# Kernel tuning notes

Hardware: AMD Instinct MI355X
Metric: run time of the kernel (lower is better)

The kernel has to match this reference:

```python
import jax, jax.numpy as jnp
import numpy as np

B, S, H = 2, 2048, 2048
NUM_HEADS, HEAD_DIM, GROUP_SIZE = 16, 128, 4
NUM_KV_HEADS = NUM_HEADS // GROUP_SIZE
ROPE_THETA = 10000.0


def setup_inputs() -> dict:
    key = jax.random.key(0)
    ks = jax.random.split(key, 10)
    xavier = lambda k, fi, fo: jax.random.uniform(k, (fi, fo), jnp.float32,
                                                  -jnp.sqrt(6.0 / (fi + fo)), jnp.sqrt(6.0 / (fi + fo)))
    hidden_states = jax.random.normal(ks[0], (B, S, H), jnp.float32)
    # causal mask: 1.0 where attention is disallowed (strictly upper triangle)
    mask = jnp.triu(jnp.ones((S, S), jnp.float32), k=1)[None, None, :, :]
    mask = jnp.broadcast_to(mask, (B, 1, S, S))
    return {
        "hidden_states": hidden_states,
        "mask": mask,
        "Wq": xavier(ks[1], H, NUM_HEADS * HEAD_DIM), "bq": jnp.zeros((NUM_HEADS * HEAD_DIM,), jnp.float32),
        "Wk": xavier(ks[2], H, NUM_KV_HEADS * HEAD_DIM), "bk": jnp.zeros((NUM_KV_HEADS * HEAD_DIM,), jnp.float32),
        "Wv": xavier(ks[3], H, NUM_KV_HEADS * HEAD_DIM), "bv": jnp.zeros((NUM_KV_HEADS * HEAD_DIM,), jnp.float32),
        "Wo": xavier(ks[4], NUM_HEADS * HEAD_DIM, H), "bo": jnp.zeros((H,), jnp.float32),
    }


def _apply_rope(q, k):
    # q: [b, s, hq, d], k: [b, s, hk, d]
    s, d = q.shape[1], q.shape[-1]
    inv_freq = 1.0 / (ROPE_THETA ** (jnp.arange(0, d, 2, dtype=jnp.float32) / d))  # [d/2]
    angles = jnp.arange(s, dtype=jnp.float32)[:, None] * inv_freq[None, :]          # [s, d/2]
    cos = jnp.cos(angles)[None, :, None, :]  # [1, s, 1, d/2]
    sin = jnp.sin(angles)[None, :, None, :]

    def rot(x):
        x1, x2 = jnp.split(x, 2, axis=-1)
        return jnp.concatenate([x1 * cos - x2 * sin, x1 * sin + x2 * cos], axis=-1)

    return rot(q), rot(k)


def reference(hidden_states, mask, Wq, bq, Wk, bk, Wv, bv, Wo, bo):
    b, s, _ = hidden_states.shape
    scale = 1.0 / jnp.sqrt(jnp.float32(HEAD_DIM))

    q = (hidden_states @ Wq + bq).reshape(b, s, NUM_HEADS, HEAD_DIM)
    k = (hidden_states @ Wk + bk).reshape(b, s, NUM_KV_HEADS, HEAD_DIM)
    v = (hidden_states @ Wv + bv).reshape(b, s, NUM_KV_HEADS, HEAD_DIM)

    q, k = _apply_rope(q, k)

    q = jnp.transpose(q, (0, 2, 1, 3))  # [b, hq, s, d]
    k = jnp.transpose(k, (0, 2, 1, 3))  # [b, hk, s, d]
    v = jnp.transpose(v, (0, 2, 1, 3))

    new_past_key, new_past_value = k, v

    # GQA: repeat each KV head group_size times
    k_rep = jnp.repeat(k, GROUP_SIZE, axis=1)  # [b, hq, s, d]
    v_rep = jnp.repeat(v, GROUP_SIZE, axis=1)

    attn_scores = jnp.einsum('bhqd,bhkd->bhqk', q, k_rep) * scale  # [b, hq, s, s]
    attn_scores = attn_scores + mask * -1e9
    attn_probs = jax.nn.softmax(attn_scores, axis=-1)
    attn_output = jnp.einsum('bhqk,bhkd->bhqd', attn_probs, v_rep)

    attn_output = attn_output.transpose(0, 2, 1, 3).reshape(b, s, NUM_HEADS * HEAD_DIM)
    attn_output = attn_output @ Wo + bo
    return attn_output, new_past_key, new_past_value
```

## Files before the change

kernel.cpp:

```cpp
#include <hip/hip_runtime.h>
#include <stdint.h>

#define S_LEN 2048
#define HDIM  2048
#define N_HEADS 16
#define HEAD_D 128
#define N_KV 4

typedef unsigned short u16;
typedef __attribute__((ext_vector_type(8))) short bf16x8;
typedef __attribute__((ext_vector_type(4))) short bf16x4;
typedef __attribute__((ext_vector_type(4))) float f32x4;

#define MFMA_PV(a, b, c) __builtin_amdgcn_mfma_f32_16x16x16bf16_1k(a, b, c, 0, 0, 0)

__device__ __forceinline__ u16 f2bf(float f) {
  unsigned u = __float_as_uint(f);
  u += 0x7FFFu + ((u >> 16) & 1u);
  return (u16)(u >> 16);
}

__device__ __forceinline__ float bf2f(u16 v) {
  return __uint_as_float(((unsigned)v) << 16);
}

__device__ __forceinline__ void gll16(void* lds, const void* gp) {
  __builtin_amdgcn_global_load_lds(
      (const __attribute__((address_space(1))) void*)gp,
      (__attribute__((address_space(3))) void*)lds, 16, 0, 0);
}

__global__ __launch_bounds__(256) void k_convert(const float* __restrict__ src,
                                                 u16* __restrict__ dst, int n4) {
  int i = blockIdx.x * 256 + threadIdx.x;
  if (i < n4) {
    float4 v = ((const float4*)src)[i];
    ushort4 o;
    o.x = f2bf(v.x); o.y = f2bf(v.y); o.z = f2bf(v.z); o.w = f2bf(v.w);
    ((ushort4*)dst)[i] = o;
  }
}

__global__ __launch_bounds__(256) void k_transpose_w(const float* __restrict__ W,
                                                     u16* __restrict__ Wt,
                                                     int K, int N) {
  __shared__ float tile[64][65];
  int k0 = blockIdx.x * 64, n0 = blockIdx.y * 64;
  int tr = threadIdx.x >> 6, tc = threadIdx.x & 63;
#pragma unroll
  for (int i = 0; i < 16; ++i) {
    int r = tr + i * 4;
    tile[r][tc] = W[(size_t)(k0 + r) * N + n0 + tc];
  }
  __syncthreads();
#pragma unroll
  for (int i = 0; i < 16; ++i) {
    int r = tr + i * 4;
    Wt[(size_t)(n0 + r) * K + k0 + tc] = f2bf(tile[tc][r]);
  }
}

__device__ __forceinline__ void gemm_tile_128(
    const u16* __restrict__ A, const u16* __restrict__ Bt,
    const float* __restrict__ bias, float* __restrict__ C,
    int m0, int n0, int K, int ldc) {
  __shared__ __align__(16) u16 sA[128 * 32];
  __shared__ __align__(16) u16 sB[128 * 32];
  const int tid = threadIdx.x;
  const int lane = tid & 63;
  const int wave = tid >> 6;
  const int quad = lane >> 4;
  const int l15 = lane & 15;
  const int wm = (wave >> 1) << 6;
  const int wn = (wave & 1) << 6;

  f32x4 acc[4][4];
#pragma unroll
  for (int i = 0; i < 4; ++i)
#pragma unroll
    for (int j = 0; j < 4; ++j)
      acc[i][j] = (f32x4){0.f, 0.f, 0.f, 0.f};

  for (int kk = 0; kk < K; kk += 32) {
    __syncthreads();
#pragma unroll
    for (int it = 0; it < 2; ++it) {
      int c = tid + (it << 8);
      int row = c >> 2;
      int ko = (c & 3) << 3;
      gll16((char*)sA + c * 16, A + (size_t)(m0 + row) * K + kk + ko);
      gll16((char*)sB + c * 16, Bt + (size_t)(n0 + row) * K + kk + ko);
    }
    __syncthreads();
    bf16x8 af[4], bfr[4];
#pragma unroll
    for (int i = 0; i < 4; ++i)
      af[i] = *(const bf16x8*)&sA[(wm + (i << 4) + l15) * 32 + quad * 8];
#pragma unroll
    for (int j = 0; j < 4; ++j)
      bfr[j] = *(const bf16x8*)&sB[(wn + (j << 4) + l15) * 32 + quad * 8];
#pragma unroll
    for (int i = 0; i < 4; ++i)
#pragma unroll
      for (int j = 0; j < 4; ++j)
        acc[i][j] = __builtin_amdgcn_mfma_f32_16x16x32_bf16(af[i], bfr[j], acc[i][j], 0, 0, 0);
  }

#pragma unroll
  for (int i = 0; i < 4; ++i) {
    int row = m0 + wm + (i << 4) + quad * 4;
#pragma unroll
    for (int j = 0; j < 4; ++j) {
      int col = n0 + wn + (j << 4) + l15;
      float bv = bias[col];
      float* cp = C + (size_t)row * ldc + col;
#pragma unroll
      for (int r = 0; r < 4; ++r)
        cp[(size_t)r * ldc] = acc[i][j][r] + bv;
    }
  }
}

__global__ __launch_bounds__(256) void k_gemm_qkv(
    const u16* __restrict__ X, const u16* __restrict__ Wqt,
    const u16* __restrict__ Wkt, const u16* __restrict__ Wvt,
    const float* __restrict__ bq, const float* __restrict__ bk,
    const float* __restrict__ bv, float* __restrict__ Qf,
    float* __restrict__ Kf, float* __restrict__ Vf) {
  int m0 = blockIdx.x << 7;
  int by = blockIdx.y;
  const u16* Bt; const float* bias; float* C; int n0, ldc;
  if (by < 16)      { Bt = Wqt; bias = bq; C = Qf; n0 = by << 7;        ldc = 2048; }
  else if (by < 20) { Bt = Wkt; bias = bk; C = Kf; n0 = (by - 16) << 7; ldc = 512;  }
  else              { Bt = Wvt; bias = bv; C = Vf; n0 = (by - 20) << 7; ldc = 512;  }
  gemm_tile_128(X, Bt, bias, C, m0, n0, 2048, ldc);
}

__global__ __launch_bounds__(256) void k_gemm_o(
    const u16* __restrict__ A, const u16* __restrict__ Wot,
    const float* __restrict__ bo, float* __restrict__ C) {
  gemm_tile_128(A, Wot, bo, C, blockIdx.x << 7, blockIdx.y << 7, 2048, 2048);
}

__global__ __launch_bounds__(256) void k_rope(
    const float* __restrict__ Qf, const float* __restrict__ Kf,
    u16* __restrict__ Qbf, u16* __restrict__ Kbf, float* __restrict__ outK) {
  const int bx = blockIdx.x;
  const int b = bx >> 11;
  const int s = bx & 2047;
  const int tid = threadIdx.x;
  const float qscale = 0.08838834764831845f * 1.4426950408889634f;
  const float c1 = -13.287712379549449f / 64.f;

#pragma unroll
  for (int it = 0; it < 4; ++it) {
    int p = tid + (it << 8);
    int hh = p >> 6;
    int ii = p & 63;
    float ang = (float)s * exp2f((float)ii * c1);
    float cs, sn;
    sincosf(ang, &sn, &cs);
    const float* src = Qf + (size_t)bx * 2048 + hh * 128 + ii;
    float x1 = src[0], x2 = src[64];
    float o1 = (x1 * cs - x2 * sn) * qscale;
    float o2 = (x1 * sn + x2 * cs) * qscale;
    u16* dst = Qbf + ((size_t)(b * N_HEADS + hh) * S_LEN + s) * HEAD_D + ii;
    dst[0] = f2bf(o1);
    dst[64] = f2bf(o2);
  }
  {
    int hh = tid >> 6;
    int ii = tid & 63;
    float ang = (float)s * exp2f((float)ii * c1);
    float cs, sn;
    sincosf(ang, &sn, &cs);
    const float* src = Kf + (size_t)bx * 512 + hh * 128 + ii;
    float x1 = src[0], x2 = src[64];
    float o1 = x1 * cs - x2 * sn;
    float o2 = x1 * sn + x2 * cs;
    size_t idx = ((size_t)(b * N_KV + hh) * S_LEN + s) * HEAD_D + ii;
    Kbf[idx] = f2bf(o1);
    Kbf[idx + 64] = f2bf(o2);
    outK[idx] = o1;
    outK[idx + 64] = o2;
  }
}

__global__ __launch_bounds__(256) void k_vtrans(const float* __restrict__ Vf,
                                                u16* __restrict__ Vt,
                                                float* __restrict__ outV) {
  __shared__ float tile[64][65];
  int s0 = blockIdx.x * 64, d0 = blockIdx.y * 64;
  int z = blockIdx.z;
  int b = z >> 2, kvh = z & 3;
  int tr = threadIdx.x >> 6, tc = threadIdx.x & 63;
#pragma unroll
  for (int i = 0; i < 16; ++i) {
    int r = tr + i * 4;
    float v = Vf[(size_t)(b * S_LEN + s0 + r) * 512 + kvh * 128 + d0 + tc];
    tile[r][tc] = v;
    outV[((size_t)z * S_LEN + s0 + r) * HEAD_D + d0 + tc] = v;
  }
  __syncthreads();
#pragma unroll
  for (int i = 0; i < 16; ++i) {
    int r = tr + i * 4;
    Vt[((size_t)z * HEAD_D + d0 + r) * S_LEN + s0 + tc] = f2bf(tile[tc][r]);
  }
}

__global__ __launch_bounds__(256, 2) void k_attn(
    const u16* __restrict__ Qbf, const u16* __restrict__ Kbf,
    const u16* __restrict__ Vt, u16* __restrict__ attn,
    u16* __restrict__ pO, float* __restrict__ pML) {
  __shared__ __align__(16) u16 smem[17920];
  u16* sK = smem;
  u16* sV = smem + 8704;

  const int tid = threadIdx.x;
  const int lane = tid & 63;
  const int wave = tid >> 6;
  const int quad = lane >> 4;
  const int l15 = lane & 15;

  const int by = blockIdx.y;
  int qt, t0, t1, slot;
  bool finalw;
  if (by < 8) {
    qt = 8 + by; t0 = 0; t1 = 16; finalw = false;
    slot = ((blockIdx.x << 3) + (qt - 8)) << 1;
  } else {
    qt = 23 - by;
    if (qt >= 8) {
      t0 = 16; t1 = 2 * qt + 2; finalw = false;
      slot = (((blockIdx.x << 3) + (qt - 8)) << 1) + 1;
    } else {
      t0 = 0; t1 = 2 * qt + 2; finalw = true; slot = 0;
    }
  }

  const int bh = blockIdx.x;
  const int b = bh >> 4;
  const int h = bh & 15;
  const int kvh = h >> 2;
  const int q0 = qt << 7;
  const int qw = q0 + wave * 32;

  const u16* Qb = Qbf + ((size_t)(b * N_HEADS + h) * S_LEN + qw) * HEAD_D;
  const u16* Kb = Kbf + (size_t)(b * N_KV + kvh) * S_LEN * HEAD_D;
  const u16* Vb = Vt + (size_t)(b * N_KV + kvh) * HEAD_D * S_LEN;

  bf16x8 aq[2][4];
#pragma unroll
  for (int i = 0; i < 2; ++i)
#pragma unroll
    for (int kc = 0; kc < 4; ++kc)
      aq[i][kc] = *(const bf16x8*)(Qb + (size_t)(i * 16 + l15) * HEAD_D + kc * 32 + quad * 8);

  float mst[2] = {-1e30f, -1e30f}, lst[2] = {0.f, 0.f};
  f32x4 oacc[2][8];
#pragma unroll
  for (int i = 0; i < 2; ++i)
#pragma unroll
    for (int n = 0; n < 8; ++n) oacc[i][n] = (f32x4){0.f, 0.f, 0.f, 0.f};

  for (int t = t0; t < t1; ++t) {
    const int kt0 = t << 6;
    __syncthreads();
#pragma unroll
    for (int it = 0; it < 9; ++it) {
      int c = tid + (it << 8);
      if (c < 1088) {
        int row = c / 17;
        int k16 = c - row * 17;
        gll16((char*)sK + c * 16, Kb + (size_t)(kt0 + row) * HEAD_D + k16 * 8);
      } else if (c < 2240) {
        int vv = c - 1088;
        int d = vv / 9;
        int s16 = vv - d * 9;
        gll16((char*)sV + vv * 16, Vb + (size_t)d * S_LEN + kt0 + s16 * 8);
      }
    }
    __syncthreads();

    if (kt0 > qw + 31) continue;

    f32x4 st[2][4];
#pragma unroll
    for (int i = 0; i < 2; ++i)
#pragma unroll
      for (int j = 0; j < 4; ++j) st[i][j] = (f32x4){0.f, 0.f, 0.f, 0.f};
#pragma unroll
    for (int kc = 0; kc < 4; ++kc) {
#pragma unroll
      for (int j = 0; j < 4; ++j) {
        bf16x8 kf = *(const bf16x8*)&sK[(j * 16 + l15) * 136 + kc * 32 + quad * 8];
#pragma unroll
        for (int i = 0; i < 2; ++i)
          st[i][j] = __builtin_amdgcn_mfma_f32_16x16x32_bf16(kf, aq[i][kc], st[i][j], 0, 0, 0);
      }
    }

    if (kt0 + 63 > qw) {
#pragma unroll
      for (int i = 0; i < 2; ++i) {
        int q = qw + i * 16 + l15;
#pragma unroll
        for (int j = 0; j < 4; ++j) {
          int s = kt0 + j * 16 + quad * 4;
#pragma unroll
          for (int r = 0; r < 4; ++r)
            if (s + r > q) st[i][j][r] = -1e9f;
        }
      }
    }

    bf16x4 pf[2][4];
    float al[2];
#pragma unroll
    for (int i = 0; i < 2; ++i) {
      float m = -1e30f;
#pragma unroll
      for (int j = 0; j < 4; ++j)
#pragma unroll
        for (int r = 0; r < 4; ++r) m = fmaxf(m, st[i][j][r]);
      m = fmaxf(m, __shfl_xor(m, 16, 64));
      m = fmaxf(m, __shfl_xor(m, 32, 64));
      float mn = fmaxf(mst[i], m);
      al[i] = exp2f(mst[i] - mn);
      mst[i] = mn;
      float rs = 0.f;
#pragma unroll
      for (int j = 0; j < 4; ++j) {
        float p0 = exp2f(st[i][j][0] - mn);
        float p1 = exp2f(st[i][j][1] - mn);
        float p2 = exp2f(st[i][j][2] - mn);
        float p3 = exp2f(st[i][j][3] - mn);
        rs += (p0 + p1) + (p2 + p3);
        union { unsigned u[2]; bf16x4 v; } pk;
        pk.u[0] = __builtin_amdgcn_perm(__float_as_uint(p1) + 0x8000u,
                                        __float_as_uint(p0) + 0x8000u, 0x07060302u);
        pk.u[1] = __builtin_amdgcn_perm(__float_as_uint(p3) + 0x8000u,
                                        __float_as_uint(p2) + 0x8000u, 0x07060302u);
        pf[i][j] = pk.v;
      }
      rs += __shfl_xor(rs, 16, 64);
      rs += __shfl_xor(rs, 32, 64);
      lst[i] = lst[i] * al[i] + rs;
#pragma unroll
      for (int r = 0; r < 4; ++r) {
        float a = __shfl(al[i], quad * 4 + r, 16);
#pragma unroll
        for (int n = 0; n < 8; ++n) oacc[i][n][r] *= a;
      }
    }

#pragma unroll
    for (int j = 0; j < 4; ++j) {
#pragma unroll
      for (int n = 0; n < 8; ++n) {
        bf16x4 vf = *(const bf16x4*)&sV[(n * 16 + l15) * 72 + j * 16 + quad * 4];
#pragma unroll
        for (int i = 0; i < 2; ++i)
          oacc[i][n] = MFMA_PV(pf[i][j], vf, oacc[i][n]);
      }
    }
  }

  if (finalw) {
#pragma unroll
    for (int i = 0; i < 2; ++i)
#pragma unroll
      for (int r = 0; r < 4; ++r) {
        float inv = 1.0f / __shfl(lst[i], quad * 4 + r, 16);
        int row = qw + i * 16 + quad * 4 + r;
        u16* op = attn + ((size_t)b * S_LEN + row) * HDIM + h * HEAD_D;
#pragma unroll
        for (int n = 0; n < 8; ++n)
          op[n * 16 + l15] = f2bf(oacc[i][n][r] * inv);
      }
  } else {
    u16* po = pO + (size_t)slot * 16384;
#pragma unroll
    for (int i = 0; i < 2; ++i)
#pragma unroll
      for (int r = 0; r < 4; ++r) {
        int row = wave * 32 + i * 16 + quad * 4 + r;
#pragma unroll
        for (int n = 0; n < 8; ++n)
          po[row * 128 + n * 16 + l15] = f2bf(oacc[i][n][r]);
      }
    if (quad == 0) {
      float* ml = pML + slot * 256;
#pragma unroll
      for (int i = 0; i < 2; ++i) {
        int row = wave * 32 + i * 16 + l15;
        ml[row] = mst[i];
        ml[128 + row] = lst[i];
      }
    }
  }
}

__global__ __launch_bounds__(256) void k_attn_combine(
    const u16* __restrict__ pO, const float* __restrict__ pML,
    u16* __restrict__ attn) {
  const int bh = blockIdx.x;
  const int qt = 8 + blockIdx.y;
  const int b = bh >> 4;
  const int h = bh & 15;
  const int s0 = ((bh << 3) + blockIdx.y) << 1;
  const int row = threadIdx.x >> 1;
  const int half = threadIdx.x & 1;

  const float* ml0 = pML + s0 * 256;
  const float* ml1 = pML + (s0 + 1) * 256;
  float m0 = ml0[row], l0 = ml0[128 + row];
  float m1 = ml1[row], l1 = ml1[128 + row];
  float m = fmaxf(m0, m1);
  float w0 = exp2f(m0 - m), w1 = exp2f(m1 - m);
  float inv = 1.0f / (l0 * w0 + l1 * w1);
  w0 *= inv; w1 *= inv;

  const u16* o0 = pO + (size_t)s0 * 16384 + row * 128 + half * 64;
  const u16* o1 = o0 + 16384;
  u16* op = attn + ((size_t)(b * S_LEN + (qt << 7) + row)) * HDIM + h * HEAD_D + half * 64;
#pragma unroll
  for (int k = 0; k < 8; ++k) {
    ushort4 a0 = ((const ushort4*)o0)[k * 2];
    ushort4 b0 = ((const ushort4*)o0)[k * 2 + 1];
    ushort4 a1 = ((const ushort4*)o1)[k * 2];
    ushort4 b1 = ((const ushort4*)o1)[k * 2 + 1];
    ushort4 ra, rb;
    ra.x = f2bf(bf2f(a0.x) * w0 + bf2f(a1.x) * w1);
    ra.y = f2bf(bf2f(a0.y) * w0 + bf2f(a1.y) * w1);
    ra.z = f2bf(bf2f(a0.z) * w0 + bf2f(a1.z) * w1);
    ra.w = f2bf(bf2f(a0.w) * w0 + bf2f(a1.w) * w1);
    rb.x = f2bf(bf2f(b0.x) * w0 + bf2f(b1.x) * w1);
    rb.y = f2bf(bf2f(b0.y) * w0 + bf2f(b1.y) * w1);
    rb.z = f2bf(bf2f(b0.z) * w0 + bf2f(b1.z) * w1);
    rb.w = f2bf(bf2f(b0.w) * w0 + bf2f(b1.w) * w1);
    ((ushort4*)op)[k * 2] = ra;
    ((ushort4*)op)[k * 2 + 1] = rb;
  }
}

extern "C" void kernel_launch(void* const* d_in, const int* in_sizes, int n_in,
                              void* d_out, int out_size, void* d_ws, size_t ws_size,
                              hipStream_t stream) {
  (void)in_sizes; (void)n_in; (void)out_size; (void)ws_size;
  const float* hs = (const float*)d_in[0];
  const float* Wq = (const float*)d_in[2];
  const float* bq = (const float*)d_in[3];
  const float* Wk = (const float*)d_in[4];
  const float* bk = (const float*)d_in[5];
  const float* Wv = (const float*)d_in[6];
  const float* bv = (const float*)d_in[7];
  const float* Wo = (const float*)d_in[8];
  const float* bo = (const float*)d_in[9];
  float* out = (float*)d_out;

  char* ws = (char*)d_ws;
  u16* Xbf   = (u16*)(ws + 0);
  u16* Wqt   = (u16*)(ws + 16777216);
  u16* Wkt   = (u16*)(ws + 25165824);
  u16* Wvt   = (u16*)(ws + 27262976);
  u16* Wot   = (u16*)(ws + 29360128);
  float* Qf  = (float*)(ws + 37748736);
  float* Kf  = (float*)(ws + 71303168);
  float* Vf  = (float*)(ws + 79691776);
  u16* Qbf   = (u16*)(ws + 88080384);
  u16* Kbf   = (u16*)(ws + 104857600);
  u16* Vtb   = (u16*)(ws + 109051904);
  u16* attnb = (u16*)(ws + 37748736);
  float* pML = (float*)(ws + 54525952);
  u16* pO    = (u16*)(ws + 71303168);

  k_convert<<<8192, 256, 0, stream>>>(hs, Xbf, 2097152);
  k_transpose_w<<<dim3(32, 32), 256, 0, stream>>>(Wq, Wqt, 2048, 2048);
  k_transpose_w<<<dim3(32, 8), 256, 0, stream>>>(Wk, Wkt, 2048, 512);
  k_transpose_w<<<dim3(32, 8), 256, 0, stream>>>(Wv, Wvt, 2048, 512);
  k_transpose_w<<<dim3(32, 32), 256, 0, stream>>>(Wo, Wot, 2048, 2048);
  k_gemm_qkv<<<dim3(32, 24), 256, 0, stream>>>(Xbf, Wqt, Wkt, Wvt, bq, bk, bv, Qf, Kf, Vf);
  k_rope<<<4096, 256, 0, stream>>>(Qf, Kf, Qbf, Kbf, out + 8388608);
  k_vtrans<<<dim3(32, 2, 8), 256, 0, stream>>>(Vf, Vtb, out + 10485760);
  k_attn<<<dim3(32, 24), 256, 0, stream>>>(Qbf, Kbf, Vtb, attnb, pO, pML);
  k_attn_combine<<<dim3(32, 8), 256, 0, stream>>>(pO, pML, attnb);
  k_gemm_o<<<dim3(32, 16), 256, 0, stream>>>(attnb, Wot, bo, out);
}
```

Before: 365.1 us.

## Double-buffer K/V tiles in attention kernel with async prefetch and wave priority

Splits the attention kernel's shared-memory staging into two buffers. The next K/V tile is issued with direct-to-LDS loads before computing on the current tile, and a partial vmcnt wait lets the previous tile land while new loads stay in flight. It also raises wave priority around the MFMA blocks with s_setprio. The cost is double the LDS per block, which may reduce the occupancy implied by launch_bounds(256,2), and the hand-counted vmcnt(8) must match the number of outstanding loads per thread.

After: 373.5 us. 1.02x slower.

```diff
diff --git a/kernel.cpp b/kernel.cpp
--- a/kernel.cpp
+++ b/kernel.cpp
@@ -213,9 +213,7 @@
     const u16* __restrict__ Qbf, const u16* __restrict__ Kbf,
     const u16* __restrict__ Vt, u16* __restrict__ attn,
     u16* __restrict__ pO, float* __restrict__ pML) {
-  __shared__ __align__(16) u16 smem[17920];
-  u16* sK = smem;
-  u16* sV = smem + 8704;
+  __shared__ __align__(16) u16 smem[2][17920];
 
   const int tid = threadIdx.x;
   const int lane = tid & 63;
@@ -264,108 +262,137 @@
 #pragma unroll
     for (int n = 0; n < 8; ++n) oacc[i][n] = (f32x4){0.f, 0.f, 0.f, 0.f};
 
+#define STAGE(buf, t)                                                        \
+  {                                                                          \
+    const int kt0_ = (t) << 6;                                               \
+    u16* sK_ = smem[buf];                                                    \
+    u16* sV_ = smem[buf] + 8704;                                             \
+    _Pragma("unroll")                                                        \
+    for (int it = 0; it < 9; ++it) {                                         \
+      int c = tid + (it << 8);                                               \
+      if (c < 1088) {                                                        \
+        int row = c / 17;                                                    \
+        int k16 = c - row * 17;                                              \
+        gll16((char*)sK_ + c * 16, Kb + (size_t)(kt0_ + row) * HEAD_D + k16 * 8); \
+      } else if (c < 2240) {                                                 \
+        int vv = c - 1088;                                                   \
+        int d = vv / 9;                                                      \
+        int s16 = vv - d * 9;                                                \
+        gll16((char*)sV_ + vv * 16, Vb + (size_t)d * S_LEN + kt0_ + s16 * 8); \
+      }                                                                      \
+    }                                                                        \
+  }
+
+  STAGE(0, t0);
+  int cur = 0;
+
   for (int t = t0; t < t1; ++t) {
     const int kt0 = t << 6;
-    __syncthreads();
-#pragma unroll
-    for (int it = 0; it < 9; ++it) {
-      int c = tid + (it << 8);
-      if (c < 1088) {
-        int row = c / 17;
-        int k16 = c - row * 17;
-        gll16((char*)sK + c * 16, Kb + (size_t)(kt0 + row) * HEAD_D + k16 * 8);
-      } else if (c < 2240) {
-        int vv = c - 1088;
-        int d = vv / 9;
-        int s16 = vv - d * 9;
-        gll16((char*)sV + vv * 16, Vb + (size_t)d * S_LEN + kt0 + s16 * 8);
-      }
+    if (t + 1 < t1) {
+      STAGE(cur ^ 1, t + 1);
+      asm volatile("s_waitcnt vmcnt(8)" ::: "memory");
+    } else {
+      asm volatile("s_waitcnt vmcnt(0)" ::: "memory");
     }
-    __syncthreads();
-
-    if (kt0 > qw + 31) continue;
-
-    f32x4 st[2][4];
-#pragma unroll
-    for (int i = 0; i < 2; ++i)
-#pragma unroll
-      for (int j = 0; j < 4; ++j) st[i][j] = (f32x4){0.f, 0.f, 0.f, 0.f};
-#pragma unroll
-    for (int kc = 0; kc < 4; ++kc) {
+    __builtin_amdgcn_sched_barrier(0);
+    __builtin_amdgcn_s_barrier();
+
+    const u16* sK = smem[cur];
+    const u16* sV = smem[cur] + 8704;
+
+    if (kt0 <= qw + 31) {
+      f32x4 st[2][4];
+#pragma unroll
+      for (int i = 0; i < 2; ++i)
+#pragma unroll
+        for (int j = 0; j < 4; ++j) st[i][j] = (f32x4){0.f, 0.f, 0.f, 0.f};
+      __builtin_amdgcn_s_setprio(1);
+#pragma unroll
+      for (int kc = 0; kc < 4; ++kc) {
+#pragma unroll
+        for (int j = 0; j < 4; ++j) {
+          bf16x8 kf = *(const bf16x8*)&sK[(j * 16 + l15) * 136 + kc * 32 + quad * 8];
+#pragma unroll
+          for (int i = 0; i < 2; ++i)
+            st[i][j] = __builtin_amdgcn_mfma_f32_16x16x32_bf16(kf, aq[i][kc], st[i][j], 0, 0, 0);
+        }
+      }
+      __builtin_amdgcn_s_setprio(0);
+
+      if (kt0 + 63 > qw) {
+#pragma unroll
+        for (int i = 0; i < 2; ++i) {
+          int q = qw + i * 16 + l15;
+#pragma unroll
+          for (int j = 0; j < 4; ++j) {
+            int s = kt0 + j * 16 + quad * 4;
+#pragma unroll
+            for (int r = 0; r < 4; ++r)
+              if (s + r > q) st[i][j][r] = -1e9f;
+          }
+        }
+      }
+
+      bf16x4 pf[2][4];
+      float al[2];
+#pragma unroll
+      for (int i = 0; i < 2; ++i) {
+        float m = -1e30f;
+#pragma unroll
+        for (int j = 0; j < 4; ++j)
+#pragma unroll
+          for (int r = 0; r < 4; ++r) m = fmaxf(m, st[i][j][r]);
+        m = fmaxf(m, __shfl_xor(m, 16, 64));
+        m = fmaxf(m, __shfl_xor(m, 32, 64));
+        float mn = fmaxf(mst[i], m);
+        al[i] = exp2f(mst[i] - mn);
+        mst[i] = mn;
+        float rs = 0.f;
+#pragma unroll
+        for (int j = 0; j < 4; ++j) {
+          float p0 = exp2f(st[i][j][0] - mn);
+          float p1 = exp2f(st[i][j][1] - mn);
+          float p2 = exp2f(st[i][j][2] - mn);
+          float p3 = exp2f(st[i][j][3] - mn);
+          rs += (p0 + p1) + (p2 + p3);
+          union { unsigned u[2]; bf16x4 v; } pk;
+          pk.u[0] = __builtin_amdgcn_perm(__float_as_uint(p1) + 0x8000u,
+                                          __float_as_uint(p0) + 0x8000u, 0x07060302u);
+          pk.u[1] = __builtin_amdgcn_perm(__float_as_uint(p3) + 0x8000u,
+                                          __float_as_uint(p2) + 0x8000u, 0x07060302u);
+          pf[i][j] = pk.v;
+        }
+        rs += __shfl_xor(rs, 16, 64);
+        rs += __shfl_xor(rs, 32, 64);
+        lst[i] = lst[i] * al[i] + rs;
+#pragma unroll
+        for (int r = 0; r < 4; ++r) {
+          float a = __shfl(al[i], quad * 4 + r, 16);
+#pragma unroll
+          for (int n = 0; n < 8; ++n) oacc[i][n][r] *= a;
+        }
+      }
+
+      __builtin_amdgcn_s_setprio(1);
 #pragma unroll
       for (int j = 0; j < 4; ++j) {
-        bf16x8 kf = *(const bf16x8*)&sK[(j * 16 + l15) * 136 + kc * 32 + quad * 8];
-#pragma unroll
-        for (int i = 0; i < 2; ++i)
-          st[i][j] = __builtin_amdgcn_mfma_f32_16x16x32_bf16(kf, aq[i][kc], st[i][j], 0, 0, 0);
-      }
+#pragma unroll
+        for (int n = 0; n < 8; ++n) {
+          bf16x4 vf = *(const bf16x4*)&sV[(n * 16 + l15) * 72 + j * 16 + quad * 4];
+#pragma unroll
+          for (int i = 0; i < 2; ++i)
+            oacc[i][n] = MFMA_PV(pf[i][j], vf, oacc[i][n]);
+        }
+      }
+      __builtin_amdgcn_s_setprio(0);
     }
 
-    if (kt0 + 63 > qw) {
-#pragma unroll
-      for (int i = 0; i < 2; ++i) {
-        int q = qw + i * 16 + l15;
-#pragma unroll
-        for (int j = 0; j < 4; ++j) {
-          int s = kt0 + j * 16 + quad * 4;
-#pragma unroll
-          for (int r = 0; r < 4; ++r)
-            if (s + r > q) st[i][j][r] = -1e9f;
-        }
-      }
-    }
-
-    bf16x4 pf[2][4];
-    float al[2];
-#pragma unroll
-    for (int i = 0; i < 2; ++i) {
-      float m = -1e30f;
-#pragma unroll
-      for (int j = 0; j < 4; ++j)
-#pragma unroll
-        for (int r = 0; r < 4; ++r) m = fmaxf(m, st[i][j][r]);
-      m = fmaxf(m, __shfl_xor(m, 16, 64));
-      m = fmaxf(m, __shfl_xor(m, 32, 64));
-      float mn = fmaxf(mst[i], m);
-      al[i] = exp2f(mst[i] - mn);
-      mst[i] = mn;
-      float rs = 0.f;
-#pragma unroll
-      for (int j = 0; j < 4; ++j) {
-        float p0 = exp2f(st[i][j][0] - mn);
-        float p1 = exp2f(st[i][j][1] - mn);
-        float p2 = exp2f(st[i][j][2] - mn);
-        float p3 = exp2f(st[i][j][3] - mn);
-        rs += (p0 + p1) + (p2 + p3);
-        union { unsigned u[2]; bf16x4 v; } pk;
-        pk.u[0] = __builtin_amdgcn_perm(__float_as_uint(p1) + 0x8000u,
-                                        __float_as_uint(p0) + 0x8000u, 0x07060302u);
-        pk.u[1] = __builtin_amdgcn_perm(__float_as_uint(p3) + 0x8000u,
-                                        __float_as_uint(p2) + 0x8000u, 0x07060302u);
-        pf[i][j] = pk.v;
-      }
-      rs += __shfl_xor(rs, 16, 64);
-      rs += __shfl_xor(rs, 32, 64);
-      lst[i] = lst[i] * al[i] + rs;
-#pragma unroll
-      for (int r = 0; r < 4; ++r) {
-        float a = __shfl(al[i], quad * 4 + r, 16);
-#pragma unroll
-        for (int n = 0; n < 8; ++n) oacc[i][n][r] *= a;
-      }
-    }
-
-#pragma unroll
-    for (int j = 0; j < 4; ++j) {
-#pragma unroll
-      for (int n = 0; n < 8; ++n) {
-        bf16x4 vf = *(const bf16x4*)&sV[(n * 16 + l15) * 72 + j * 16 + quad * 4];
-#pragma unroll
-        for (int i = 0; i < 2; ++i)
-          oacc[i][n] = MFMA_PV(pf[i][j], vf, oacc[i][n]);
-      }
-    }
-  }
+    asm volatile("s_waitcnt lgkmcnt(0)" ::: "memory");
+    __builtin_amdgcn_sched_barrier(0);
+    __builtin_amdgcn_s_barrier();
+    cur ^= 1;
+  }
+#undef STAGE
 
   if (finalw) {
 #pragma unroll
```

## Fuse RoPE into QKV GEMM epilogue via permuted weight columns

Applied to the files above, without the earlier changes.

The Q and K weight transposes now permute output columns so that each wave's accumulator holds matching rotary pairs (d and d+64). The QKV GEMM epilogue then applies bias, RoPE and the Q scale directly and writes the bf16 Q/K and fp32 K output. This removes the separate rope kernel and the fp32 Q/K intermediate round trip through memory. In exchange the epilogue does per-element sincos and scattered 2-byte stores, which may raise register pressure and lower store efficiency.

New measurement: 400.0 us. 9.6% more time.

```diff
diff --git a/kernel.cpp b/kernel.cpp
--- a/kernel.cpp
+++ b/kernel.cpp
@@ -43,7 +43,7 @@
 
 __global__ __launch_bounds__(256) void k_transpose_w(const float* __restrict__ W,
                                                      u16* __restrict__ Wt,
-                                                     int K, int N) {
+                                                     int K, int N, int perm) {
   __shared__ float tile[64][65];
   int k0 = blockIdx.x * 64, n0 = blockIdx.y * 64;
   int tr = threadIdx.x >> 6, tc = threadIdx.x & 63;
@@ -56,14 +56,16 @@
 #pragma unroll
   for (int i = 0; i < 16; ++i) {
     int r = tr + i * 4;
-    Wt[(size_t)(n0 + r) * K + k0 + tc] = f2bf(tile[tc][r]);
-  }
-}
-
-__device__ __forceinline__ void gemm_tile_128(
+    int nn = n0 + r;
+    if (perm)
+      nn = (nn & ~127) | ((nn & 15) | ((nn & 48) << 1) | ((nn & 64) >> 2));
+    Wt[(size_t)nn * K + k0 + tc] = f2bf(tile[tc][r]);
+  }
+}
+
+__device__ __forceinline__ void gemm_main_128(
     const u16* __restrict__ A, const u16* __restrict__ Bt,
-    const float* __restrict__ bias, float* __restrict__ C,
-    int m0, int n0, int K, int ldc) {
+    int m0, int n0, int K, f32x4 (&acc)[4][4]) {
   __shared__ __align__(16) u16 sA[128 * 32];
   __shared__ __align__(16) u16 sB[128 * 32];
   const int tid = threadIdx.x;
@@ -74,7 +76,6 @@
   const int wm = (wave >> 1) << 6;
   const int wn = (wave & 1) << 6;
 
-  f32x4 acc[4][4];
 #pragma unroll
   for (int i = 0; i < 4; ++i)
 #pragma unroll
@@ -105,6 +106,22 @@
       for (int j = 0; j < 4; ++j)
         acc[i][j] = __builtin_amdgcn_mfma_f32_16x16x32_bf16(af[i], bfr[j], acc[i][j], 0, 0, 0);
   }
+}
+
+__device__ __forceinline__ void gemm_tile_128(
+    const u16* __restrict__ A, const u16* __restrict__ Bt,
+    const float* __restrict__ bias, float* __restrict__ C,
+    int m0, int n0, int K, int ldc) {
+  const int tid = threadIdx.x;
+  const int lane = tid & 63;
+  const int wave = tid >> 6;
+  const int quad = lane >> 4;
+  const int l15 = lane & 15;
+  const int wm = (wave >> 1) << 6;
+  const int wn = (wave & 1) << 6;
+
+  f32x4 acc[4][4];
+  gemm_main_128(A, Bt, m0, n0, K, acc);
 
 #pragma unroll
   for (int i = 0; i < 4; ++i) {
@@ -121,69 +138,109 @@
   }
 }
 
-__global__ __launch_bounds__(256) void k_gemm_qkv(
+__global__ __launch_bounds__(256) void k_gemm_qkv_fused(
     const u16* __restrict__ X, const u16* __restrict__ Wqt,
     const u16* __restrict__ Wkt, const u16* __restrict__ Wvt,
     const float* __restrict__ bq, const float* __restrict__ bk,
-    const float* __restrict__ bv, float* __restrict__ Qf,
-    float* __restrict__ Kf, float* __restrict__ Vf) {
-  int m0 = blockIdx.x << 7;
-  int by = blockIdx.y;
-  const u16* Bt; const float* bias; float* C; int n0, ldc;
-  if (by < 16)      { Bt = Wqt; bias = bq; C = Qf; n0 = by << 7;        ldc = 2048; }
-  else if (by < 20) { Bt = Wkt; bias = bk; C = Kf; n0 = (by - 16) << 7; ldc = 512;  }
-  else              { Bt = Wvt; bias = bv; C = Vf; n0 = (by - 20) << 7; ldc = 512;  }
-  gemm_tile_128(X, Bt, bias, C, m0, n0, 2048, ldc);
+    const float* __restrict__ bv, u16* __restrict__ Qbf,
+    u16* __restrict__ Kbf, float* __restrict__ outK,
+    float* __restrict__ Vf) {
+  const int m0 = blockIdx.x << 7;
+  const int by = blockIdx.y;
+  const int tid = threadIdx.x;
+  const int lane = tid & 63;
+  const int wave = tid >> 6;
+  const int quad = lane >> 4;
+  const int l15 = lane & 15;
+  const int wm = (wave >> 1) << 6;
+  const int wn = (wave & 1) << 6;
+
+  const u16* Bt; int n0;
+  if (by < 16)      { Bt = Wqt; n0 = by << 7; }
+  else if (by < 20) { Bt = Wkt; n0 = (by - 16) << 7; }
+  else              { Bt = Wvt; n0 = (by - 20) << 7; }
+
+  f32x4 acc[4][4];
+  gemm_main_128(X, Bt, m0, n0, 2048, acc);
+
+  const float c1 = -13.287712379549449f / 64.f;
+
+  if (by < 16) {
+    const float qscale = 0.08838834764831845f * 1.4426950408889634f;
+    const int h = by;
+#pragma unroll
+    for (int jp = 0; jp < 2; ++jp) {
+      const int d1 = (((wn >> 5) + jp) << 4) + l15;
+      const float b1 = bq[h * 128 + d1];
+      const float b2 = bq[h * 128 + d1 + 64];
+      const float fr = exp2f((float)d1 * c1);
+#pragma unroll
+      for (int i = 0; i < 4; ++i) {
+        const int rowb = m0 + wm + (i << 4) + quad * 4;
+#pragma unroll
+        for (int r = 0; r < 4; ++r) {
+          const int tok = rowb + r;
+          const int b = tok >> 11, s = tok & 2047;
+          float sn, cs;
+          sincosf((float)s * fr, &sn, &cs);
+          float x1 = acc[i][2 * jp][r] + b1;
+          float x2 = acc[i][2 * jp + 1][r] + b2;
+          u16* dst = Qbf + ((size_t)(b * N_HEADS + h) * S_LEN + s) * HEAD_D + d1;
+          dst[0]  = f2bf((x1 * cs - x2 * sn) * qscale);
+          dst[64] = f2bf((x1 * sn + x2 * cs) * qscale);
+        }
+      }
+    }
+  } else if (by < 20) {
+    const int kvh = by - 16;
+#pragma unroll
+    for (int jp = 0; jp < 2; ++jp) {
+      const int d1 = (((wn >> 5) + jp) << 4) + l15;
+      const float b1 = bk[kvh * 128 + d1];
+      const float b2 = bk[kvh * 128 + d1 + 64];
+      const float fr = exp2f((float)d1 * c1);
+#pragma unroll
+      for (int i = 0; i < 4; ++i) {
+        const int rowb = m0 + wm + (i << 4) + quad * 4;
+#pragma unroll
+        for (int r = 0; r < 4; ++r) {
+          const int tok = rowb + r;
+          const int b = tok >> 11, s = tok & 2047;
+          float sn, cs;
+          sincosf((float)s * fr, &sn, &cs);
+          float x1 = acc[i][2 * jp][r] + b1;
+          float x2 = acc[i][2 * jp + 1][r] + b2;
+          float o1 = x1 * cs - x2 * sn;
+          float o2 = x1 * sn + x2 * cs;
+          size_t idx = ((size_t)(b * N_KV + kvh) * S_LEN + s) * HEAD_D + d1;
+          Kbf[idx]      = f2bf(o1);
+          Kbf[idx + 64] = f2bf(o2);
+          outK[idx]      = o1;
+          outK[idx + 64] = o2;
+        }
+      }
+    }
+  } else {
+#pragma unroll
+    for (int i = 0; i < 4; ++i) {
+      int row = m0 + wm + (i << 4) + quad * 4;
+#pragma unroll
+      for (int j = 0; j < 4; ++j) {
+        int col = n0 + wn + (j << 4) + l15;
+        float bvv = bv[col];
+        float* cp = Vf + (size_t)row * 512 + col;
+#pragma unroll
+        for (int r = 0; r < 4; ++r)
+          cp[(size_t)r * 512] = acc[i][j][r] + bvv;
+      }
+    }
+  }
 }
 
 __global__ __launch_bounds__(256) void k_gemm_o(
     const u16* __restrict__ A, const u16* __restrict__ Wot,
     const float* __restrict__ bo, float* __restrict__ C) {
   gemm_tile_128(A, Wot, bo, C, blockIdx.x << 7, blockIdx.y << 7, 2048, 2048);
-}
-
-__global__ __launch_bounds__(256) void k_rope(
-    const float* __restrict__ Qf, const float* __restrict__ Kf,
-    u16* __restrict__ Qbf, u16* __restrict__ Kbf, float* __restrict__ outK) {
-  const int bx = blockIdx.x;
-  const int b = bx >> 11;
-  const int s = bx & 2047;
-  const int tid = threadIdx.x;
-  const float qscale = 0.08838834764831845f * 1.4426950408889634f;
-  const float c1 = -13.287712379549449f / 64.f;
-
-#pragma unroll
-  for (int it = 0; it < 4; ++it) {
-    int p = tid + (it << 8);
-    int hh = p >> 6;
-    int ii = p & 63;
-    float ang = (float)s * exp2f((float)ii * c1);
-    float cs, sn;
-    sincosf(ang, &sn, &cs);
-    const float* src = Qf + (size_t)bx * 2048 + hh * 128 + ii;
-    float x1 = src[0], x2 = src[64];
-    float o1 = (x1 * cs - x2 * sn) * qscale;
-    float o2 = (x1 * sn + x2 * cs) * qscale;
-    u16* dst = Qbf + ((size_t)(b * N_HEADS + hh) * S_LEN + s) * HEAD_D + ii;
-    dst[0] = f2bf(o1);
-    dst[64] = f2bf(o2);
-  }
-  {
-    int hh = tid >> 6;
-    int ii = tid & 63;
-    float ang = (float)s * exp2f((float)ii * c1);
-    float cs, sn;
-    sincosf(ang, &sn, &cs);
-    const float* src = Kf + (size_t)bx * 512 + hh * 128 + ii;
-    float x1 = src[0], x2 = src[64];
-    float o1 = x1 * cs - x2 * sn;
-    float o2 = x1 * sn + x2 * cs;
-    size_t idx = ((size_t)(b * N_KV + hh) * S_LEN + s) * HEAD_D + ii;
-    Kbf[idx] = f2bf(o1);
-    Kbf[idx + 64] = f2bf(o2);
-    outK[idx] = o1;
-    outK[idx + 64] = o2;
-  }
 }
 
 __global__ __launch_bounds__(256) void k_vtrans(const float* __restrict__ Vf,
@@ -466,8 +523,6 @@
   u16* Wkt   = (u16*)(ws + 25165824);
   u16* Wvt   = (u16*)(ws + 27262976);
   u16* Wot   = (u16*)(ws + 29360128);
-  float* Qf  = (float*)(ws + 37748736);
-  float* Kf  = (float*)(ws + 71303168);
   float* Vf  = (float*)(ws + 79691776);
   u16* Qbf   = (u16*)(ws + 88080384);
   u16* Kbf   = (u16*)(ws + 104857600);
@@ -477,12 +532,12 @@
   u16* pO    = (u16*)(ws + 71303168);
 
   k_convert<<<8192, 256, 0, stream>>>(hs, Xbf, 2097152);
-  k_transpose_w<<<dim3(32, 32), 256, 0, stream>>>(Wq, Wqt, 2048, 2048);
-  k_transpose_w<<<dim3(32, 8), 256, 0, stream>>>(Wk, Wkt, 2048, 512);
-  k_transpose_w<<<dim3(32, 8), 256, 0, stream>>>(Wv, Wvt, 2048, 512);
-  k_transpose_w<<<dim3(32, 32), 256, 0, stream>>>(Wo, Wot, 2048, 2048);
-  k_gemm_qkv<<<dim3(32, 24), 256, 0, stream>>>(Xbf, Wqt, Wkt, Wvt, bq, bk, bv, Qf, Kf, Vf);
-  k_rope<<<4096, 256, 0, stream>>>(Qf, Kf, Qbf, Kbf, out + 8388608);
+  k_transpose_w<<<dim3(32, 32), 256, 0, stream>>>(Wq, Wqt, 2048, 2048, 1);
+  k_transpose_w<<<dim3(32, 8), 256, 0, stream>>>(Wk, Wkt, 2048, 512, 1);
+  k_transpose_w<<<dim3(32, 8), 256, 0, stream>>>(Wv, Wvt, 2048, 512, 0);
+  k_transpose_w<<<dim3(32, 32), 256, 0, stream>>>(Wo, Wot, 2048, 2048, 0);
+  k_gemm_qkv_fused<<<dim3(32, 24), 256, 0, stream>>>(
+      Xbf, Wqt, Wkt, Wvt, bq, bk, bv, Qbf, Kbf, out + 8388608, Vf);
   k_vtrans<<<dim3(32, 2, 8), 256, 0, stream>>>(Vf, Vtb, out + 10485760);
   k_attn<<<dim3(32, 24), 256, 0, stream>>>(Qbf, Kbf, Vtb, attnb, pO, pML);
   k_attn_combine<<<dim3(32, 8), 256, 0, stream>>>(pO, pML, attnb);
```
